# Kernel tuning notes

Hardware: AMD Instinct MI355X
Metric: run time of the kernel (lower is better)

Reference implementation:

```python
import jax, jax.numpy as jnp
import numpy as np

B, N, D, M, P = 8, 4096, 512, 512, 1
NUM_STEPS = 4
EPS = 1e-5


def _layer_norm(x, g, b):
    mu = jnp.mean(x, axis=-1, keepdims=True)
    var = jnp.mean(jnp.square(x - mu), axis=-1, keepdims=True)
    return (x - mu) * jax.lax.rsqrt(var + EPS) * g + b


def setup_inputs() -> dict:
    key = jax.random.key(0)
    ks = jax.random.split(key, 8)
    x = jax.random.normal(ks[0], (B, N, D), dtype=jnp.float32)
    positions = jax.random.uniform(ks[1], (B, N, P), dtype=jnp.float32)
    # uniform grid on [0,1], as in _generate_grid_points
    grid_points = jnp.broadcast_to(jnp.linspace(0.0, 1.0, M, dtype=jnp.float32)[None, :, None], (B, M, P))
    sc = 1.0 / np.sqrt(D).astype(np.float32)
    return {
        "x": x,
        "positions": positions,
        "grid_points": grid_points,
        "log_sigma": jnp.asarray(-2.3, jnp.float32),   # RBF bandwidth sigma ~ 0.1
        "alpha": jnp.asarray(0.1, jnp.float32),        # diffusion coefficient
        "W_int": jax.random.normal(ks[2], (D, D), jnp.float32) * sc * 0.1,  # interference mixing
        "b_int": jnp.zeros((D,), jnp.float32),
        "ln1_g": jnp.ones((D,), jnp.float32),
        "ln1_b": jnp.zeros((D,), jnp.float32),
        "W_out": jax.random.normal(ks[3], (D, D), jnp.float32) * sc,
        "b_out": jnp.zeros((D,), jnp.float32),
        "ln2_g": jnp.ones((D,), jnp.float32),
        "ln2_b": jnp.zeros((D,), jnp.float32),
    }


def reference(x, positions, grid_points, log_sigma, alpha, W_int, b_int,
              ln1_g, ln1_b, W_out, b_out, ln2_g, ln2_b):
    # ---- FieldProjector: RBF token -> grid projection ----
    sigma = jnp.exp(log_sigma)
    diff = grid_points[:, :, None, :] - positions[:, None, :, :]      # [B,M,N,P]
    sq = jnp.sum(diff * diff, axis=-1)                                # [B,M,N]
    kern = jnp.exp(-sq / (2.0 * sigma * sigma))                       # [B,M,N]
    field = jnp.einsum('bmn,bnd->bmd', kern, x)                       # [B,M,D]

    # ---- UnifiedFieldDynamics: diffusion evolution + standard interference ----
    dt = 1.0 / NUM_STEPS
    for _ in range(NUM_STEPS):
        fp = jnp.pad(field, ((0, 0), (1, 1), (0, 0)), mode='edge')    # Neumann boundary
        lap = fp[:, :-2] - 2.0 * field + fp[:, 2:]                    # 1D Laplacian on grid
        inter = jnp.tanh(field @ W_int + b_int)                       # nonlinear interference
        field = field + dt * (alpha * lap + inter)

    # ---- FieldSampler (mode='linear'): grid -> token linear interpolation ----
    u = positions[..., 0] * (M - 1)                                   # [B,N]
    i0 = jnp.clip(jnp.floor(u).astype(jnp.int32), 0, M - 2)
    w = (u - i0.astype(u.dtype))[..., None]                           # [B,N,1]
    idx0 = jnp.broadcast_to(i0[:, :, None], (B, N, D))
    f0 = jnp.take_along_axis(field, idx0, axis=1)
    f1 = jnp.take_along_axis(field, idx0 + 1, axis=1)
    sampled = (1.0 - w) * f0 + w * f1                                 # [B,N,D]

    # ---- residual + LN + Linear + residual + LN ----
    enhanced = _layer_norm(sampled + x, ln1_g, ln1_b)
    out = enhanced @ W_out + b_out
    return _layer_norm(out + enhanced, ln2_g, ln2_b)
```

## Files before the change

### kernel.cpp

```cpp
#include <hip/hip_runtime.h>
#include <cmath>

#define B_ 8
#define N_ 4096
#define D_ 512
#define M_ 512
#define EPS_ 1e-5f
#define DT_ 0.25f

typedef unsigned short u16;
typedef unsigned int u32;
typedef __attribute__((ext_vector_type(8))) u16 u16x8;
typedef __attribute__((ext_vector_type(4))) u16 u16x4;
typedef __attribute__((ext_vector_type(8))) short bf16x8;
typedef __attribute__((ext_vector_type(4))) float f32x4;

__device__ __forceinline__ float bf2f(u16 h) {
    return __builtin_bit_cast(float, (u32)h << 16);
}
__device__ __forceinline__ u32 cvtpk(float lo, float hi) {
    u32 r;
    asm("v_cvt_pk_bf16_f32 %0, %1, %2" : "=v"(r) : "v"(lo), "v"(hi));
    return r;
}
__device__ __forceinline__ u16 f2bf(float f) { return (u16)cvtpk(f, 0.f); }
__device__ __forceinline__ u16x8 pack8(float4 a, float4 b) {
    union { u32 w[4]; u16x8 o; } u;
    u.w[0] = cvtpk(a.x, a.y); u.w[1] = cvtpk(a.z, a.w);
    u.w[2] = cvtpk(b.x, b.y); u.w[3] = cvtpk(b.z, b.w);
    return u.o;
}

__device__ __forceinline__ void gload16(const void* g, void* l) {
    __builtin_amdgcn_global_load_lds(
        (const __attribute__((address_space(1))) void*)g,
        (__attribute__((address_space(3))) void*)l, 16, 0, 0);
}

__global__ __launch_bounds__(256)
void k_prep_T(const float* __restrict__ src, u16* __restrict__ dst, int R, int C)
{
    __shared__ float tile[64][65];
    const int t = threadIdx.x;
    const int c0 = blockIdx.x * 64;
    const int r0 = blockIdx.y * 64;
    const int z  = blockIdx.z;
    const float* s = src + (size_t)z * R * C;
    u16* d = dst + (size_t)z * R * C;
    const int rl = t >> 4, cc = (t & 15) * 4;
#pragma unroll
    for (int i = 0; i < 4; ++i) {
        float4 v = *reinterpret_cast<const float4*>(s + (size_t)(r0 + rl + i * 16) * C + c0 + cc);
        tile[rl + i * 16][cc + 0] = v.x;
        tile[rl + i * 16][cc + 1] = v.y;
        tile[rl + i * 16][cc + 2] = v.z;
        tile[rl + i * 16][cc + 3] = v.w;
    }
    __syncthreads();
#pragma unroll
    for (int i = 0; i < 2; ++i) {
        int q = t + i * 256;
        int cl = q >> 3, rc = (q & 7) * 8;
        float4 va, vb;
        va.x = tile[rc + 0][cl]; va.y = tile[rc + 1][cl];
        va.z = tile[rc + 2][cl]; va.w = tile[rc + 3][cl];
        vb.x = tile[rc + 4][cl]; vb.y = tile[rc + 5][cl];
        vb.z = tile[rc + 6][cl]; vb.w = tile[rc + 7][cl];
        *reinterpret_cast<u16x8*>(d + (size_t)(c0 + cl) * R + r0 + rc) = pack8(va, vb);
    }
}

__global__ __launch_bounds__(512, 4)
void k_projgemm(const float* __restrict__ pos, const float* __restrict__ gp,
                const float* __restrict__ log_sigma, const u16* __restrict__ xT,
                float* __restrict__ field)
{
    extern __shared__ u16 smem[];
    u16* As = smem;
    u16* Bs = smem + 64 * 64;

    const int t = threadIdx.x;
    const int d = blockIdx.x;
    const int xcd = d & 7;
    const int q = d >> 3;
    const int w = q & 15;
    const int mtile = w & 7;
    const int ntile = w >> 3;
    const int gq = q >> 4;
    const int g = gq * 8 + xcd;
    const int b = g & 7;
    const int m0 = mtile * 64;
    const int cb0 = ntile * 256;
    const int nc0 = (g >> 3) * 1024;

    const int l = t & 63, wid = t >> 6;
    const int wm = wid >> 2, wn = wid & 3;

    f32x4 acc[2][4];
#pragma unroll
    for (int i = 0; i < 2; ++i)
#pragma unroll
        for (int j = 0; j < 4; ++j) acc[i][j] = (f32x4){0.f, 0.f, 0.f, 0.f};

    const int a_row = t >> 3, a_sch = t & 7;
    const int a_gch = a_sch ^ (a_row & 7);
    const float gm = gp[(size_t)b * M_ + m0 + a_row];
    const float sigma = __expf(log_sigma[0]);
    const float ninv2s2 = -0.5f / (sigma * sigma);
    const float* pb = pos + (size_t)b * N_ + nc0 + a_gch * 8;
    u16* a_wr = As + a_row * 64 + a_sch * 8;

    const u16* xb = xT + ((size_t)b * D_ + cb0) * N_ + nc0;

    const int fr = l & 15, fj = l >> 4;

    for (int ks = 0; ks < 16; ++ks) {
        const int kk = ks * 64;
        __syncthreads();
#pragma unroll
        for (int i = 0; i < 4; ++i) {
            const int cid = t + i * 512;
            const int brow = cid >> 3, bsch = cid & 7;
            gload16(xb + (size_t)brow * N_ + kk + ((bsch ^ (brow & 7)) * 8),
                    Bs + (size_t)wid * 512 + i * 4096);
        }
        {
            float4 p0 = *reinterpret_cast<const float4*>(pb + kk);
            float4 p1 = *reinterpret_cast<const float4*>(pb + kk + 4);
            float4 ea, eb;
            float d0 = gm - p0.x, d1 = gm - p0.y, d2 = gm - p0.z, d3 = gm - p0.w;
            float d4 = gm - p1.x, d5 = gm - p1.y, d6 = gm - p1.z, d7 = gm - p1.w;
            ea.x = __expf(d0 * d0 * ninv2s2); ea.y = __expf(d1 * d1 * ninv2s2);
            ea.z = __expf(d2 * d2 * ninv2s2); ea.w = __expf(d3 * d3 * ninv2s2);
            eb.x = __expf(d4 * d4 * ninv2s2); eb.y = __expf(d5 * d5 * ninv2s2);
            eb.z = __expf(d6 * d6 * ninv2s2); eb.w = __expf(d7 * d7 * ninv2s2);
            *reinterpret_cast<u16x8*>(a_wr) = pack8(ea, eb);
        }
        __syncthreads();

#pragma unroll
        for (int kl = 0; kl < 2; ++kl) {
            const int cbase = kl * 4 + fj;
            const int ar0 = wm * 32 + fr, ar1 = ar0 + 16;
            bf16x8 a0 = *reinterpret_cast<const bf16x8*>(
                As + ar0 * 64 + ((cbase ^ (ar0 & 7)) * 8));
            bf16x8 a1 = *reinterpret_cast<const bf16x8*>(
                As + ar1 * 64 + ((cbase ^ (ar1 & 7)) * 8));
#pragma unroll
            for (int nf = 0; nf < 4; ++nf) {
                const int bcol = wn * 64 + nf * 16 + fr;
                bf16x8 bw = *reinterpret_cast<const bf16x8*>(
                    Bs + bcol * 64 + ((cbase ^ (bcol & 7)) * 8));
                acc[0][nf] = __builtin_amdgcn_mfma_f32_16x16x32_bf16(a0, bw, acc[0][nf], 0, 0, 0);
                acc[1][nf] = __builtin_amdgcn_mfma_f32_16x16x32_bf16(a1, bw, acc[1][nf], 0, 0, 0);
            }
        }
    }

    float* fb = field + (size_t)b * M_ * D_;
#pragma unroll
    for (int mf = 0; mf < 2; ++mf)
#pragma unroll
        for (int nf = 0; nf < 4; ++nf) {
            const int col = cb0 + wn * 64 + nf * 16 + fr;
#pragma unroll
            for (int r = 0; r < 4; ++r) {
                const int m = m0 + wm * 32 + mf * 16 + fj * 4 + r;
                unsafeAtomicAdd(fb + (size_t)m * D_ + col, acc[mf][nf][r]);
            }
        }
}

__global__ __launch_bounds__(256, 8)
void k_diffuse(const float* __restrict__ fin, const u16* __restrict__ WiT,
               const float* __restrict__ bi, const float* __restrict__ alpha_p,
               float* __restrict__ fout)
{
    extern __shared__ u16 dsm[];
    u16* fs = dsm;
    u16* Bs = dsm + 16 * 520;
    float* Cs = (float*)Bs;

    const int t = threadIdx.x;
    const int m0 = blockIdx.x * 16;
    const int cb0 = blockIdx.y * 256;
    const int b = blockIdx.z;
    const int l = t & 63, wn = t >> 6;
    const int fr = l & 15, fj = l >> 4;
    const float* fb = fin + (size_t)b * M_ * D_;

    {
        const int row = t >> 4, ch = (t & 15) * 32;
        const float* src = fb + (size_t)(m0 + row) * D_ + ch;
#pragma unroll
        for (int j = 0; j < 4; ++j) {
            float4 v0 = *reinterpret_cast<const float4*>(src + j * 8);
            float4 v1 = *reinterpret_cast<const float4*>(src + j * 8 + 4);
            *reinterpret_cast<u16x8*>(fs + row * 520 + ch + j * 8) = pack8(v0, v1);
        }
    }

    f32x4 acc[4];
#pragma unroll
    for (int i = 0; i < 4; ++i) acc[i] = (f32x4){0.f, 0.f, 0.f, 0.f};

    const u16* wb = WiT + (size_t)cb0 * D_;

    for (int ks = 0; ks < 8; ++ks) {
        const int kk = ks * 64;
        __syncthreads();
#pragma unroll
        for (int i = 0; i < 8; ++i) {
            const int cid = t + i * 256;
            const int brow = cid >> 3, bsch = cid & 7;
            gload16(wb + (size_t)brow * D_ + kk + ((bsch ^ (brow & 7)) * 8),
                    Bs + (i * 256 + wn * 64) * 8);
        }
        __syncthreads();

#pragma unroll
        for (int kl = 0; kl < 2; ++kl) {
            const int cbase = kl * 4 + fj;
            bf16x8 a = *reinterpret_cast<const bf16x8*>(
                fs + fr * 520 + kk + kl * 32 + fj * 8);
#pragma unroll
            for (int nf = 0; nf < 4; ++nf) {
                const int bcol = wn * 64 + nf * 16 + fr;
                bf16x8 bw = *reinterpret_cast<const bf16x8*>(
                    Bs + bcol * 64 + ((cbase ^ (bcol & 7)) * 8));
                acc[nf] = __builtin_amdgcn_mfma_f32_16x16x32_bf16(a, bw, acc[nf], 0, 0, 0);
            }
        }
    }

    __syncthreads();
#pragma unroll
    for (int nf = 0; nf < 4; ++nf) {
        const int cl = wn * 64 + nf * 16 + fr;
        const float bic = bi[cb0 + cl];
#pragma unroll
        for (int r = 0; r < 4; ++r)
            Cs[(fj * 4 + r) * 260 + cl] = acc[nf][r] + bic;
    }
    __syncthreads();

    const float al = alpha_p[0];
    float* fob = fout + (size_t)b * M_ * D_;
#pragma unroll
    for (int i = 0; i < 4; ++i) {
        const int row = wn * 4 + i;
        const int m = m0 + row;
        const int mu_ = m > 0 ? m - 1 : 0;
        const int md = m < M_ - 1 ? m + 1 : M_ - 1;
        const int cl = cb0 + l * 4;
        float4 g  = *reinterpret_cast<const float4*>(&Cs[row * 260 + l * 4]);
        float4 fc = *reinterpret_cast<const float4*>(fb + (size_t)m * D_ + cl);
        float4 fu = *reinterpret_cast<const float4*>(fb + (size_t)mu_ * D_ + cl);
        float4 fd = *reinterpret_cast<const float4*>(fb + (size_t)md * D_ + cl);
        float4 o;
        o.x = fc.x + DT_ * (al * (fu.x + fd.x - 2.f * fc.x) + tanhf(g.x));
        o.y = fc.y + DT_ * (al * (fu.y + fd.y - 2.f * fc.y) + tanhf(g.y));
        o.z = fc.z + DT_ * (al * (fu.z + fd.z - 2.f * fc.z) + tanhf(g.z));
        o.w = fc.w + DT_ * (al * (fu.w + fd.w - 2.f * fc.w) + tanhf(g.w));
        *reinterpret_cast<float4*>(fob + (size_t)m * D_ + cl) = o;
    }
}

__global__ __launch_bounds__(256)
void k_enh(const float* __restrict__ x, const float* __restrict__ pos,
           const float* __restrict__ field, const float* __restrict__ g1,
           const float* __restrict__ b1, u16* __restrict__ enh)
{
    const int t = threadIdx.x;
    const int wid = t >> 6, l = t & 63;
    const int n = blockIdx.x * 4 + wid;
    const int b = blockIdx.y;
    const int c = l * 8;

    const float* xr = x + ((size_t)b * N_ + n) * D_ + c;
    float4 xa = *reinterpret_cast<const float4*>(xr);
    float4 xb = *reinterpret_cast<const float4*>(xr + 4);
    const float p = pos[(size_t)b * N_ + n];
    float u = p * (float)(M_ - 1);
    int i0 = (int)floorf(u);
    i0 = i0 < 0 ? 0 : (i0 > M_ - 2 ? M_ - 2 : i0);
    const float w = u - (float)i0;
    const float* fp0 = field + ((size_t)b * M_ + i0) * D_ + c;
    float4 f0a = *reinterpret_cast<const float4*>(fp0);
    float4 f0b = *reinterpret_cast<const float4*>(fp0 + 4);
    float4 f1a = *reinterpret_cast<const float4*>(fp0 + D_);
    float4 f1b = *reinterpret_cast<const float4*>(fp0 + D_ + 4);

    float s[8];
    s[0] = f0a.x + w * (f1a.x - f0a.x) + xa.x;
    s[1] = f0a.y + w * (f1a.y - f0a.y) + xa.y;
    s[2] = f0a.z + w * (f1a.z - f0a.z) + xa.z;
    s[3] = f0a.w + w * (f1a.w - f0a.w) + xa.w;
    s[4] = f0b.x + w * (f1b.x - f0b.x) + xb.x;
    s[5] = f0b.y + w * (f1b.y - f0b.y) + xb.y;
    s[6] = f0b.z + w * (f1b.z - f0b.z) + xb.z;
    s[7] = f0b.w + w * (f1b.w - f0b.w) + xb.w;

    float sum = 0.f, ss = 0.f;
#pragma unroll
    for (int j = 0; j < 8; ++j) { sum += s[j]; ss += s[j] * s[j]; }
#pragma unroll
    for (int off = 1; off <= 32; off <<= 1) {
        sum += __shfl_xor(sum, off);
        ss  += __shfl_xor(ss, off);
    }
    const float mu = sum * (1.f / 512.f);
    const float rs = rsqrtf(ss * (1.f / 512.f) - mu * mu + EPS_);

    float4 ga = *reinterpret_cast<const float4*>(g1 + c);
    float4 gb = *reinterpret_cast<const float4*>(g1 + c + 4);
    float4 ba = *reinterpret_cast<const float4*>(b1 + c);
    float4 bb = *reinterpret_cast<const float4*>(b1 + c + 4);
    float4 ea, eb;
    ea.x = (s[0] - mu) * rs * ga.x + ba.x;
    ea.y = (s[1] - mu) * rs * ga.y + ba.y;
    ea.z = (s[2] - mu) * rs * ga.z + ba.z;
    ea.w = (s[3] - mu) * rs * ga.w + ba.w;
    eb.x = (s[4] - mu) * rs * gb.x + bb.x;
    eb.y = (s[5] - mu) * rs * gb.y + bb.y;
    eb.z = (s[6] - mu) * rs * gb.z + bb.z;
    eb.w = (s[7] - mu) * rs * gb.w + bb.w;
    *reinterpret_cast<u16x8*>(enh + ((size_t)b * N_ + n) * D_ + c) = pack8(ea, eb);
}

__global__ __launch_bounds__(512, 4)
void k_gemm_ln(const u16* __restrict__ enh, const u16* __restrict__ WoT,
               const float* __restrict__ bo, const float* __restrict__ g2,
               const float* __restrict__ b2, float* __restrict__ out)
{
    extern __shared__ u16 smem[];
    u16* As = smem;
    u16* Bs = smem + 64 * 64;
    float* Cs = (float*)smem;

    const int t = threadIdx.x;
    const int r0 = blockIdx.x * 64;
    const int l = t & 63, wid = t >> 6;
    const int wm = wid >> 2, wn = wid & 3;

    f32x4 acc[2][8];
#pragma unroll
    for (int i = 0; i < 2; ++i)
#pragma unroll
        for (int j = 0; j < 8; ++j) acc[i][j] = (f32x4){0.f, 0.f, 0.f, 0.f};

    const int a_row = t >> 3, a_sch = t & 7;
    const u16* a_src = enh + (size_t)(r0 + a_row) * D_ + (a_sch ^ (a_row & 7)) * 8;
    u16* a_dst = As + (size_t)wid * 512;

    const int fr = l & 15, fj = l >> 4;

    for (int ks = 0; ks < 8; ++ks) {
        const int kk = ks * 64;
        __syncthreads();
        gload16(a_src + kk, a_dst);
#pragma unroll
        for (int i = 0; i < 8; ++i) {
            const int cid = t + i * 512;
            const int brow = cid >> 3, bsch = cid & 7;
            gload16(WoT + (size_t)brow * D_ + kk + ((bsch ^ (brow & 7)) * 8),
                    Bs + (size_t)wid * 512 + i * 4096);
        }
        __syncthreads();

#pragma unroll
        for (int kl = 0; kl < 2; ++kl) {
            const int cbase = kl * 4 + fj;
            const int ar0 = wm * 32 + fr, ar1 = ar0 + 16;
            bf16x8 a0 = *reinterpret_cast<const bf16x8*>(
                As + ar0 * 64 + ((cbase ^ (ar0 & 7)) * 8));
            bf16x8 a1 = *reinterpret_cast<const bf16x8*>(
                As + ar1 * 64 + ((cbase ^ (ar1 & 7)) * 8));
#pragma unroll
            for (int nf = 0; nf < 8; ++nf) {
                const int bcol = wn * 128 + nf * 16 + fr;
                bf16x8 bw = *reinterpret_cast<const bf16x8*>(
                    Bs + bcol * 64 + ((cbase ^ (bcol & 7)) * 8));
                acc[0][nf] = __builtin_amdgcn_mfma_f32_16x16x32_bf16(a0, bw, acc[0][nf], 0, 0, 0);
                acc[1][nf] = __builtin_amdgcn_mfma_f32_16x16x32_bf16(a1, bw, acc[1][nf], 0, 0, 0);
            }
        }
    }

#pragma unroll
    for (int mf = 0; mf < 2; ++mf) {
        __syncthreads();
#pragma unroll
        for (int nf = 0; nf < 8; ++nf) {
            const int col = wn * 128 + nf * 16 + fr;
            const float boc = bo[col];
#pragma unroll
            for (int r = 0; r < 4; ++r)
                Cs[(wm * 16 + fj * 4 + r) * 516 + col] = acc[mf][nf][r] + boc;
        }
        __syncthreads();
#pragma unroll
        for (int i = 0; i < 4; ++i) {
            const int lr = wid * 4 + i;
            const int grow = r0 + (lr >> 4) * 32 + mf * 16 + (lr & 15);
            const int c1 = l * 4, c2 = 256 + l * 4;
            float4 fa = *reinterpret_cast<const float4*>(&Cs[lr * 516 + c1]);
            float4 fb4 = *reinterpret_cast<const float4*>(&Cs[lr * 516 + c2]);
            u16x4 e1 = *reinterpret_cast<const u16x4*>(enh + (size_t)grow * D_ + c1);
            u16x4 e2 = *reinterpret_cast<const u16x4*>(enh + (size_t)grow * D_ + c2);
            float v[8];
            v[0] = fa.x + bf2f(e1[0]); v[1] = fa.y + bf2f(e1[1]);
            v[2] = fa.z + bf2f(e1[2]); v[3] = fa.w + bf2f(e1[3]);
            v[4] = fb4.x + bf2f(e2[0]); v[5] = fb4.y + bf2f(e2[1]);
            v[6] = fb4.z + bf2f(e2[2]); v[7] = fb4.w + bf2f(e2[3]);

            float sum = 0.f, ss = 0.f;
#pragma unroll
            for (int j = 0; j < 8; ++j) { sum += v[j]; ss += v[j] * v[j]; }
#pragma unroll
            for (int off = 1; off <= 32; off <<= 1) {
                sum += __shfl_xor(sum, off);
                ss  += __shfl_xor(ss, off);
            }
            const float mu = sum * (1.f / 512.f);
            const float rs = rsqrtf(ss * (1.f / 512.f) - mu * mu + EPS_);

            float4 ga = *reinterpret_cast<const float4*>(g2 + c1);
            float4 gb = *reinterpret_cast<const float4*>(g2 + c2);
            float4 ba = *reinterpret_cast<const float4*>(b2 + c1);
            float4 bb = *reinterpret_cast<const float4*>(b2 + c2);
            float4 oa, ob;
            oa.x = (v[0] - mu) * rs * ga.x + ba.x;
            oa.y = (v[1] - mu) * rs * ga.y + ba.y;
            oa.z = (v[2] - mu) * rs * ga.z + ba.z;
            oa.w = (v[3] - mu) * rs * ga.w + ba.w;
            ob.x = (v[4] - mu) * rs * gb.x + bb.x;
            ob.y = (v[5] - mu) * rs * gb.y + bb.y;
            ob.z = (v[6] - mu) * rs * gb.z + bb.z;
            ob.w = (v[7] - mu) * rs * gb.w + bb.w;
            float* orow = out + (size_t)grow * D_;
            *reinterpret_cast<float4*>(orow + c1) = oa;
            *reinterpret_cast<float4*>(orow + c2) = ob;
        }
    }
}

extern "C" void kernel_launch(void* const* d_in, const int* in_sizes, int n_in,
                              void* d_out, int out_size, void* d_ws, size_t ws_size,
                              hipStream_t stream) {
    (void)in_sizes; (void)n_in; (void)out_size; (void)ws_size;
    const float* x   = (const float*)d_in[0];
    const float* pos = (const float*)d_in[1];
    const float* gp  = (const float*)d_in[2];
    const float* ls  = (const float*)d_in[3];
    const float* al  = (const float*)d_in[4];
    const float* Wi  = (const float*)d_in[5];
    const float* bi  = (const float*)d_in[6];
    const float* g1  = (const float*)d_in[7];
    const float* b1  = (const float*)d_in[8];
    const float* Wo  = (const float*)d_in[9];
    const float* bo  = (const float*)d_in[10];
    const float* g2  = (const float*)d_in[11];
    const float* b2  = (const float*)d_in[12];
    float* out = (float*)d_out;

    float* f0 = (float*)d_ws;
    float* f1 = f0 + (size_t)B_ * M_ * D_;
    u16* xT  = (u16*)(f1 + (size_t)B_ * M_ * D_);
    u16* WiT = xT + (size_t)B_ * D_ * N_;
    u16* WoT = WiT + (size_t)D_ * D_;
    u16* enh = xT;

    const int smGemm = 64 * 64 * 2 + 512 * 64 * 2;
    const int smProj = 64 * 64 * 2 + 256 * 64 * 2;
    const int smDiff = 16 * 520 * 2 + 256 * 64 * 2;
    hipFuncSetAttribute(reinterpret_cast<const void*>(k_gemm_ln),
                        hipFuncAttributeMaxDynamicSharedMemorySize, smGemm);
    hipFuncSetAttribute(reinterpret_cast<const void*>(k_projgemm),
                        hipFuncAttributeMaxDynamicSharedMemorySize, smProj);
    hipFuncSetAttribute(reinterpret_cast<const void*>(k_diffuse),
                        hipFuncAttributeMaxDynamicSharedMemorySize, smDiff);

    hipMemsetAsync(f0, 0, (size_t)B_ * M_ * D_ * sizeof(float), stream);
    k_prep_T<<<dim3(D_ / 64, N_ / 64, B_), 256, 0, stream>>>(x, xT, N_, D_);
    k_prep_T<<<dim3(D_ / 64, D_ / 64, 1), 256, 0, stream>>>(Wi, WiT, D_, D_);
    k_prep_T<<<dim3(D_ / 64, D_ / 64, 1), 256, 0, stream>>>(Wo, WoT, D_, D_);
    k_projgemm<<<dim3(512), 512, smProj, stream>>>(pos, gp, ls, xT, f0);
    k_diffuse<<<dim3(M_ / 16, D_ / 256, B_), 256, smDiff, stream>>>(f0, WiT, bi, al, f1);
    k_diffuse<<<dim3(M_ / 16, D_ / 256, B_), 256, smDiff, stream>>>(f1, WiT, bi, al, f0);
    k_diffuse<<<dim3(M_ / 16, D_ / 256, B_), 256, smDiff, stream>>>(f0, WiT, bi, al, f1);
    k_diffuse<<<dim3(M_ / 16, D_ / 256, B_), 256, smDiff, stream>>>(f1, WiT, bi, al, f0);
    k_enh<<<dim3(N_ / 4, B_), 256, 0, stream>>>(x, pos, f0, g1, b1, enh);
    k_gemm_ln<<<dim3(B_ * N_ / 64), 512, smGemm, stream>>>(enh, WoT, bo, g2, b2, out);
}
```

Before: 182.7 us.

## Replace atomic split-K accumulation with partial buffers and separate reduction kernel

The projection GEMM now writes split-K partial results with plain stores into four partial buffers, placed in the output buffer as scratch, instead of atomically adding into a zeroed field. A new kernel sums the four partials into the field, and the memset is dropped. The column tile is halved so the grid doubles to 1024 blocks, giving more parallelism. This avoids atomic contention and the memset, at the cost of extra memory traffic and one more launch.

```diff
diff --git a/kernel.cpp b/kernel.cpp
--- a/kernel.cpp
+++ b/kernel.cpp
@@ -73,7 +73,7 @@
 __global__ __launch_bounds__(512, 4)
 void k_projgemm(const float* __restrict__ pos, const float* __restrict__ gp,
                 const float* __restrict__ log_sigma, const u16* __restrict__ xT,
-                float* __restrict__ field)
+                float* __restrict__ part)
 {
     extern __shared__ u16 smem[];
     u16* As = smem;
@@ -83,24 +83,25 @@
     const int d = blockIdx.x;
     const int xcd = d & 7;
     const int q = d >> 3;
-    const int w = q & 15;
+    const int w = q & 31;
     const int mtile = w & 7;
     const int ntile = w >> 3;
-    const int gq = q >> 4;
+    const int gq = q >> 5;
     const int g = gq * 8 + xcd;
     const int b = g & 7;
+    const int kc = g >> 3;
     const int m0 = mtile * 64;
-    const int cb0 = ntile * 256;
-    const int nc0 = (g >> 3) * 1024;
+    const int cb0 = ntile * 128;
+    const int nc0 = kc * 1024;
 
     const int l = t & 63, wid = t >> 6;
     const int wm = wid >> 2, wn = wid & 3;
 
-    f32x4 acc[2][4];
+    f32x4 acc[2][2];
 #pragma unroll
     for (int i = 0; i < 2; ++i)
 #pragma unroll
-        for (int j = 0; j < 4; ++j) acc[i][j] = (f32x4){0.f, 0.f, 0.f, 0.f};
+        for (int j = 0; j < 2; ++j) acc[i][j] = (f32x4){0.f, 0.f, 0.f, 0.f};
 
     const int a_row = t >> 3, a_sch = t & 7;
     const int a_gch = a_sch ^ (a_row & 7);
@@ -118,7 +119,7 @@
         const int kk = ks * 64;
         __syncthreads();
 #pragma unroll
-        for (int i = 0; i < 4; ++i) {
+        for (int i = 0; i < 2; ++i) {
             const int cid = t + i * 512;
             const int brow = cid >> 3, bsch = cid & 7;
             gload16(xb + (size_t)brow * N_ + kk + ((bsch ^ (brow & 7)) * 8),
@@ -147,8 +148,8 @@
             bf16x8 a1 = *reinterpret_cast<const bf16x8*>(
                 As + ar1 * 64 + ((cbase ^ (ar1 & 7)) * 8));
 #pragma unroll
-            for (int nf = 0; nf < 4; ++nf) {
-                const int bcol = wn * 64 + nf * 16 + fr;
+            for (int nf = 0; nf < 2; ++nf) {
+                const int bcol = wn * 32 + nf * 16 + fr;
                 bf16x8 bw = *reinterpret_cast<const bf16x8*>(
                     Bs + bcol * 64 + ((cbase ^ (bcol & 7)) * 8));
                 acc[0][nf] = __builtin_amdgcn_mfma_f32_16x16x32_bf16(a0, bw, acc[0][nf], 0, 0, 0);
@@ -157,18 +158,35 @@
         }
     }
 
-    float* fb = field + (size_t)b * M_ * D_;
+    float* pb_out = part + ((size_t)(kc * B_ + b) * M_) * D_;
 #pragma unroll
     for (int mf = 0; mf < 2; ++mf)
 #pragma unroll
-        for (int nf = 0; nf < 4; ++nf) {
-            const int col = cb0 + wn * 64 + nf * 16 + fr;
+        for (int nf = 0; nf < 2; ++nf) {
+            const int col = cb0 + wn * 32 + nf * 16 + fr;
 #pragma unroll
             for (int r = 0; r < 4; ++r) {
                 const int m = m0 + wm * 32 + mf * 16 + fj * 4 + r;
-                unsafeAtomicAdd(fb + (size_t)m * D_ + col, acc[mf][nf][r]);
+                pb_out[(size_t)m * D_ + col] = acc[mf][nf][r];
             }
         }
+}
+
+__global__ __launch_bounds__(256)
+void k_sum(const float* __restrict__ part, float* __restrict__ field)
+{
+    const size_t i = ((size_t)blockIdx.x * 256 + threadIdx.x) * 4;
+    const size_t S = (size_t)B_ * M_ * D_;
+    float4 v0 = *reinterpret_cast<const float4*>(part + i);
+    float4 v1 = *reinterpret_cast<const float4*>(part + S + i);
+    float4 v2 = *reinterpret_cast<const float4*>(part + 2 * S + i);
+    float4 v3 = *reinterpret_cast<const float4*>(part + 3 * S + i);
+    float4 o;
+    o.x = (v0.x + v1.x) + (v2.x + v3.x);
+    o.y = (v0.y + v1.y) + (v2.y + v3.y);
+    o.z = (v0.z + v1.z) + (v2.z + v3.z);
+    o.w = (v0.w + v1.w) + (v2.w + v3.w);
+    *reinterpret_cast<float4*>(field + i) = o;
 }
 
 __global__ __launch_bounds__(256, 8)
@@ -470,9 +488,10 @@
     u16* WiT = xT + (size_t)B_ * D_ * N_;
     u16* WoT = WiT + (size_t)D_ * D_;
     u16* enh = xT;
+    float* part = (float*)d_out;
 
     const int smGemm = 64 * 64 * 2 + 512 * 64 * 2;
-    const int smProj = 64 * 64 * 2 + 256 * 64 * 2;
+    const int smProj = 64 * 64 * 2 + 128 * 64 * 2;
     const int smDiff = 16 * 520 * 2 + 256 * 64 * 2;
     hipFuncSetAttribute(reinterpret_cast<const void*>(k_gemm_ln),
                         hipFuncAttributeMaxDynamicSharedMemorySize, smGemm);
@@ -481,11 +500,11 @@
     hipFuncSetAttribute(reinterpret_cast<const void*>(k_diffuse),
                         hipFuncAttributeMaxDynamicSharedMemorySize, smDiff);
 
-    hipMemsetAsync(f0, 0, (size_t)B_ * M_ * D_ * sizeof(float), stream);
     k_prep_T<<<dim3(D_ / 64, N_ / 64, B_), 256, 0, stream>>>(x, xT, N_, D_);
     k_prep_T<<<dim3(D_ / 64, D_ / 64, 1), 256, 0, stream>>>(Wi, WiT, D_, D_);
     k_prep_T<<<dim3(D_ / 64, D_ / 64, 1), 256, 0, stream>>>(Wo, WoT, D_, D_);
-    k_projgemm<<<dim3(512), 512, smProj, stream>>>(pos, gp, ls, xT, f0);
+    k_projgemm<<<dim3(1024), 512, smProj, stream>>>(pos, gp, ls, xT, part);
+    k_sum<<<dim3((B_ * M_ * D_) / (256 * 4)), 256, 0, stream>>>(part, f0);
     k_diffuse<<<dim3(M_ / 16, D_ / 256, B_), 256, smDiff, stream>>>(f0, WiT, bi, al, f1);
     k_diffuse<<<dim3(M_ / 16, D_ / 256, B_), 256, smDiff, stream>>>(f1, WiT, bi, al, f0);
     k_diffuse<<<dim3(M_ / 16, D_ / 256, B_), 256, smDiff, stream>>>(f0, WiT, bi, al, f1);
```

Result: faster. 167.0 us (-8.6%).
